# Kernel tuning notes

Measured on AMD Instinct MI355X. Metric: run time of the kernel, lower is better.

The kernel has to match this reference:

```python
import jax, jax.numpy as jnp
import numpy as np

B, T, I, H, L = 128, 2048, 4, 400, 20


def setup_inputs() -> dict:
    key = jax.random.key(0)
    ks = jax.random.split(key, 18)
    p = lambda k, shape: (jax.random.normal(k, shape, jnp.float32) * 0.05)
    return {
        "x": jax.random.normal(ks[0], (B, T, I), jnp.float32),
        "eps": jax.random.normal(ks[1], (B, L), jnp.float32),
        # encoder LSTM (input 4 -> hidden 400); torch gate order i,f,g,o; b = b_ih+b_hh
        "W_enc_ih": p(ks[2], (4 * H, I)),
        "W_enc_hh": p(ks[3], (4 * H, H)),
        "b_enc": p(ks[4], (4 * H,)),
        "W_mu": p(ks[5], (L, H)), "b_mu": p(ks[6], (L,)),
        "W_lv": p(ks[7], (L, H)), "b_lv": p(ks[8], (L,)),
        # latent -> decoder initial hidden (decoder hidden size = I = 4)
        "W_l2h": p(ks[9], (I, L)), "b_l2h": p(ks[10], (I,)),
        # input_to_hidden: 4 -> 400
        "W_i2h": p(ks[11], (H, I)), "b_i2h": p(ks[12], (H,)),
        # decoder LSTM (input 400 -> hidden 4)
        "W_dec_ih": p(ks[13], (4 * I, H)),
        "W_dec_hh": p(ks[14], (4 * I, I)),
        "b_dec": p(ks[15], (4 * I,)),
    }


def _lstm_last(xw, W_hh, h0, c0):
    # xw: [B, T, 4Hd] precomputed input-to-gate projections (+bias)
    def step(carry, xw_t):
        h, c = carry
        g = xw_t + h @ W_hh.T
        i, f, gg, o = jnp.split(g, 4, axis=-1)
        c = jax.nn.sigmoid(f) * c + jax.nn.sigmoid(i) * jnp.tanh(gg)
        h = jax.nn.sigmoid(o) * jnp.tanh(c)
        return (h, c), None
    (h, c), _ = jax.lax.scan(step, (h0, c0), jnp.swapaxes(xw, 0, 1))
    return h


def reference(x, eps, W_enc_ih, W_enc_hh, b_enc, W_mu, b_mu, W_lv, b_lv,
              W_l2h, b_l2h, W_i2h, b_i2h, W_dec_ih, W_dec_hh, b_dec):
    b = x.shape[0]
    # ---- encode ----
    xw = jnp.einsum('bti,gi->btg', x, W_enc_ih) + b_enc  # [B,T,4H]
    h0 = jnp.zeros((b, H), x.dtype)
    last = _lstm_last(xw, W_enc_hh, h0, h0)              # [B,H] == lstm_out[:, -1]
    mu = last @ W_mu.T + b_mu                            # [B,L]
    logvar = last @ W_lv.T + b_lv                        # [B,L]
    # ---- reparameterize ----
    z = mu + eps * jnp.exp(0.5 * logvar)                 # [B,L]
    # ---- decode (teacher-forced per-step loop -> fused scan) ----
    u = jax.nn.relu(jnp.einsum('bti,hi->bth', x, W_i2h) + b_i2h)  # [B,T,H]
    uw = jnp.einsum('bth,gh->btg', u, W_dec_ih) + b_dec            # [B,T,4I]
    hd0 = z @ W_l2h.T + b_l2h                                      # [B,I]
    cd0 = jnp.zeros((b, I), x.dtype)
    sample = _lstm_last(uw, W_dec_hh, hd0, cd0)                    # [B,I] last-step output
    return sample, mu, logvar
```

## Files before the change

kernel.cpp:

```cpp
#include <hip/hip_runtime.h>
#include <cstdint>

#define T_STEPS 2048
#define BPG 16
#define HROW 416
#define KCH 13
#define NPOS (128 * 2048)
#define POLL_CAP 16384

typedef float f32x4 __attribute__((ext_vector_type(4)));
typedef short s16x8 __attribute__((ext_vector_type(8)));
typedef unsigned int u32x4 __attribute__((ext_vector_type(4)));

__device__ __forceinline__ unsigned int f2bf(float f) {
  unsigned int u = __float_as_uint(f);
  return (u + 0x7FFFu + ((u >> 16) & 1u)) >> 16;
}
__device__ __forceinline__ float sigm(float x) { return 1.0f / (1.0f + __expf(-x)); }
__device__ __forceinline__ float tanh_f(float x) { return 1.0f - 2.0f / (__expf(2.0f * x) + 1.0f); }

#define DPPF(x, ctrl) __int_as_float(__builtin_amdgcn_update_dpp(0, __float_as_int(x), (ctrl), 0xf, 0xf, true))

__device__ __forceinline__ float gate_update(const f32x4 m, const int q, float& c_st) {
  const bool q0 = (q & 1), q1b = (q & 2);
  float sA = DPPF(q0 ? m[0] : m[1], 0xB1);
  float sB = DPPF(q0 ? m[2] : m[3], 0xB1);
  float n0 = q0 ? sA : m[0];
  float n1 = q0 ? m[1] : sA;
  float n2 = q0 ? sB : m[2];
  float n3 = q0 ? m[3] : sB;
  float tA = DPPF(q1b ? n0 : n2, 0x4E);
  float tB = DPPF(q1b ? n1 : n3, 0x4E);
  float g0 = q1b ? tA : n0;
  float g1 = q1b ? tB : n1;
  float g2 = q1b ? n2 : tA;
  float g3 = q1b ? n3 : tB;
  float cn = sigm(g1) * c_st + sigm(g0) * tanh_f(g2);
  c_st = cn;
  return sigm(g3) * tanh_f(cn);
}

__device__ __forceinline__ void st_sys_b128(void* p, u32x4 v) {
  asm volatile("global_store_dwordx4 %0, %1, off sc0 sc1" :: "v"(p), "v"(v) : "memory");
}

__global__ __launch_bounds__(320, 2) void enc_uw_kernel(
    const float* __restrict__ x, const float* __restrict__ W_hh,
    const float* __restrict__ W_ih, const float* __restrict__ b_enc,
    unsigned short* __restrict__ hbuf, float* __restrict__ last_h,
    int* __restrict__ ctrl,
    const float* __restrict__ W_i2h, const float* __restrict__ b_i2h,
    const float* __restrict__ W_dec, const float* __restrict__ b_dec,
    float* __restrict__ uw)
{
  __shared__ char smem[33664];
  const int tid = threadIdx.x;
  const int bid = blockIdx.x;

  if (bid >= 80) {
    float4* Wi = (float4*)smem;
    float4 (*WdT)[4] = (float4(*)[4])(smem + 6400);
    float* bi = (float*)(smem + 32000);
    float* bd = (float*)(smem + 33600);
    for (int i = tid; i < 400; i += 320) {
      Wi[i] = *(const float4*)(W_i2h + (size_t)i * 4);
      bi[i] = b_i2h[i];
    }
    for (int i = tid; i < 6400; i += 320) {
      int gq = i & 15, hh = i >> 4;
      ((float*)&WdT[hh][0])[gq] = W_dec[(size_t)gq * 400 + hh];
    }
    if (tid < 16) bd[tid] = b_dec[tid];
    __syncthreads();
#pragma unroll
    for (int rep = 0; rep < 2; ++rep) {
      const int pos = (bid - 80) * 640 + rep * 320 + tid;
      if (pos < NPOS) {
        float4 xv = *(const float4*)(x + (size_t)pos * 4);
        float a[16];
#pragma unroll
        for (int qq = 0; qq < 16; ++qq) a[qq] = bd[qq];
        for (int hh = 0; hh < 400; ++hh) {
          float4 wv = Wi[hh];
          float u = fmaxf(wv.x * xv.x + wv.y * xv.y + wv.z * xv.z + wv.w * xv.w + bi[hh], 0.f);
#pragma unroll
          for (int q4 = 0; q4 < 4; ++q4) {
            float4 d = WdT[hh][q4];
            a[q4 * 4 + 0] = fmaf(d.x, u, a[q4 * 4 + 0]);
            a[q4 * 4 + 1] = fmaf(d.y, u, a[q4 * 4 + 1]);
            a[q4 * 4 + 2] = fmaf(d.z, u, a[q4 * 4 + 2]);
            a[q4 * 4 + 3] = fmaf(d.w, u, a[q4 * 4 + 3]);
          }
        }
        float4* o = (float4*)(uw + (size_t)pos * 16);
#pragma unroll
        for (int q4 = 0; q4 < 4; ++q4)
          o[q4] = make_float4(a[q4 * 4], a[q4 * 4 + 1], a[q4 * 4 + 2], a[q4 * 4 + 3]);
      }
    }
    return;
  }

  const int g = bid & 7, s = bid >> 3;
  const int wave = tid >> 6, lane = tid & 63;
  const int bbase = g * BPG;
  const int o = s * 5 + wave;
  const int cw = lane & 15, kgrp = lane >> 4;
  const int q = lane & 3, a = (lane >> 2) & 3;
  const int gate = cw & 3, uloc = cw >> 2;
  const int ubase = 8 * o;
  const int batch = 4 * kgrp + q;
  int* tagsG = ctrl + g * 64;

  const int perm[8] = {0, 4, 1, 5, 2, 6, 3, 7};
  s16x8 bv0[KCH], bv1[KCH];
#pragma unroll
  for (int tt = 0; tt < 2; ++tt) {
    const int row = gate * 400 + ubase + tt * 4 + uloc;
    const float* wr = W_hh + (size_t)row * 400;
#pragma unroll
    for (int kc = 0; kc < KCH; ++kc) {
      s16x8 bb;
#pragma unroll
      for (int i = 0; i < 8; ++i) {
        const int gk = kc * 32 + kgrp * 8 + i;
        float w;
        if (gk < 400)      w = wr[(size_t)(kc * 4 + kgrp) * 8 + perm[i]];
        else if (gk < 404) w = W_ih[(size_t)row * 4 + (gk - 400)];
        else               w = 0.f;
        bb[i] = (short)f2bf(w);
      }
      if (tt == 0) bv0[kc] = bb; else bv1[kc] = bb;
    }
  }
  const float bias0 = b_enc[gate * 400 + ubase + uloc];
  const float bias1 = b_enc[gate * 400 + ubase + 4 + uloc];

  if (s == 0 && wave == 0 && a == 0) {
    float4 xv = *(const float4*)(x + (size_t)(bbase + batch) * T_STEPS * 4);
    u32x4 xp = {f2bf(xv.x) | (f2bf(xv.y) << 16), f2bf(xv.z) | (f2bf(xv.w) << 16), 0u, 0u};
    st_sys_b128((char*)(hbuf + (size_t)(bbase + batch) * HROW) + 800, xp);
  }
  asm volatile("s_waitcnt vmcnt(0)" ::: "memory");
  __syncthreads();
  if (wave == 0 && lane == 0)
    __hip_atomic_store(&tagsG[s], 1, __ATOMIC_RELAXED, __HIP_MEMORY_SCOPE_AGENT);

  float c0 = 0.f, c1 = 0.f;

  for (int t = 0; t < T_STEPS; ++t) {
    const int p = t & 1;
    float4 xn;
    const bool do_x = (s == 0) && (wave == 0) && (a == 0) && (t + 1 < T_STEPS);
    if (do_x) xn = *(const float4*)(x + ((size_t)(bbase + batch) * T_STEPS + (t + 1)) * 4);

    {
      const int tgt = t + 1;
      const unsigned long long* tp = (const unsigned long long*)tagsG;
      int iter = 0;
      bool ok;
      do {
        unsigned long long v = ~0ull;
        if (lane < 5)
          v = __hip_atomic_load(&tp[lane], __ATOMIC_RELAXED, __HIP_MEMORY_SCOPE_AGENT);
        ok = (lane >= 5) || (((int)(unsigned int)v >= tgt) && ((int)(v >> 32) >= tgt));
        if (++iter > POLL_CAP) break;
      } while (!__all(ok));
    }

    {
      char* dst = smem + p * 13312;
      const char* src = (const char*)(hbuf + ((size_t)p * 128 + bbase) * HROW);
      const int i0 = tid, i1 = tid + 320, i2 = tid + 640;
      const int r0 = i0 / 52, col0 = i0 % 52;
      const int r1 = i1 / 52, col1 = i1 % 52;
      const int r2 = i2 / 52, col2 = i2 % 52;
      const bool h2 = i2 < 832;
      u32x4 v0, v1, v2;
      asm volatile("global_load_dwordx4 %0, %1, off sc0 sc1"
                   : "=v"(v0) : "v"(src + r0 * 832 + col0 * 16) : "memory");
      asm volatile("global_load_dwordx4 %0, %1, off sc0 sc1"
                   : "=v"(v1) : "v"(src + r1 * 832 + col1 * 16) : "memory");
      if (h2)
        asm volatile("global_load_dwordx4 %0, %1, off sc0 sc1"
                     : "=v"(v2) : "v"(src + r2 * 832 + col2 * 16) : "memory");
      asm volatile("s_waitcnt vmcnt(0)" ::: "memory");
      *(u32x4*)(dst + r0 * 832 + col0 * 16) = v0;
      *(u32x4*)(dst + r1 * 832 + col1 * 16) = v1;
      if (h2) *(u32x4*)(dst + r2 * 832 + col2 * 16) = v2;
    }
    __syncthreads();

    const char* At = smem + p * 13312 + cw * 832 + kgrp * 16;
    s16x8 av[KCH];
#pragma unroll
    for (int kc = 0; kc < KCH; ++kc) av[kc] = *(const s16x8*)(At + kc * 64);

    f32x4 acc00 = {bias0, bias0, bias0, bias0};
    f32x4 acc01 = {0.f, 0.f, 0.f, 0.f};
    f32x4 acc10 = {bias1, bias1, bias1, bias1};
    f32x4 acc11 = {0.f, 0.f, 0.f, 0.f};
#define MM(i)                                                                    \
    if ((i) & 1) {                                                               \
      acc01 = __builtin_amdgcn_mfma_f32_16x16x32_bf16(av[i], bv0[i], acc01, 0, 0, 0); \
      acc11 = __builtin_amdgcn_mfma_f32_16x16x32_bf16(av[i], bv1[i], acc11, 0, 0, 0); \
    } else {                                                                     \
      acc00 = __builtin_amdgcn_mfma_f32_16x16x32_bf16(av[i], bv0[i], acc00, 0, 0, 0); \
      acc10 = __builtin_amdgcn_mfma_f32_16x16x32_bf16(av[i], bv1[i], acc10, 0, 0, 0); \
    }
    MM(0) MM(1) MM(2) MM(3) MM(4) MM(5) MM(6) MM(7) MM(8) MM(9) MM(10) MM(11) MM(12)
#undef MM
    f32x4 m0 = acc00 + acc01;
    f32x4 m1 = acc10 + acc11;

    float hn0 = gate_update(m0, q, c0);
    float hn1 = gate_update(m1, q, c1);

    unsigned int v32 = f2bf(hn0) | (f2bf(hn1) << 16);
    const int srcb = lane & 51;
    unsigned int w0 = (unsigned int)__shfl((int)v32, srcb);
    unsigned int w1 = (unsigned int)__shfl((int)v32, srcb + 4);
    unsigned int w2 = (unsigned int)__shfl((int)v32, srcb + 8);
    unsigned int w3 = (unsigned int)__shfl((int)v32, srcb + 12);
    if (a == 0) {
      char* rp = (char*)(hbuf + ((size_t)(p ^ 1) * 128 + bbase + batch) * HROW) + o * 16;
      u32x4 val = {w0, w1, w2, w3};
      st_sys_b128(rp, val);
      if (do_x) {
        u32x4 xp = {f2bf(xn.x) | (f2bf(xn.y) << 16), f2bf(xn.z) | (f2bf(xn.w) << 16), 0u, 0u};
        st_sys_b128(rp - o * 16 + 800, xp);
      }
    }
    if (t == T_STEPS - 1) {
      float* lp = last_h + (size_t)(bbase + batch) * 400 + ubase;
      lp[a] = hn0;
      lp[4 + a] = hn1;
    }
    asm volatile("s_waitcnt vmcnt(0)" ::: "memory");
    __syncthreads();
    if (wave == 0 && lane == 0)
      __hip_atomic_store(&tagsG[s], t + 2, __ATOMIC_RELAXED, __HIP_MEMORY_SCOPE_AGENT);
  }
}

__global__ __launch_bounds__(64) void head_dec_kernel(
    const float* __restrict__ last_h, const float* __restrict__ eps,
    const float* __restrict__ W_mu, const float* __restrict__ b_mu,
    const float* __restrict__ W_lv, const float* __restrict__ b_lv,
    const float* __restrict__ W_l2h, const float* __restrict__ b_l2h,
    const float* __restrict__ Whh, const float* __restrict__ uw,
    float* __restrict__ out)
{
  const int b = blockIdx.x, tid = threadIdx.x;
  __shared__ float smu[20], slv[20], sz[20], hd4[4];
  const float4* h4 = (const float4*)(last_h + (size_t)b * 400);
  if (tid < 40) {
    const int o = tid % 20;
    const float4* w4 = (const float4*)((tid < 20 ? W_mu : W_lv) + (size_t)o * 400);
    float s = 0.f;
#pragma unroll 4
    for (int k = 0; k < 100; ++k) {
      float4 a = h4[k], w = w4[k];
      s += a.x * w.x + a.y * w.y + a.z * w.z + a.w * w.w;
    }
    if (tid < 20) { s += b_mu[o]; smu[o] = s; out[512 + b * 20 + o] = s; }
    else          { s += b_lv[o]; slv[o] = s; out[512 + 2560 + b * 20 + o] = s; }
  }
  __syncthreads();
  if (tid < 20) sz[tid] = smu[tid] + eps[b * 20 + tid] * __expf(0.5f * slv[tid]);
  __syncthreads();
  if (tid < 4) {
    float s = b_l2h[tid];
    for (int l = 0; l < 20; ++l) s += W_l2h[tid * 20 + l] * sz[l];
    hd4[tid] = s;
  }
  __syncthreads();
  if (tid < 4) {
    const int j = tid;
    float w[4][4];
#pragma unroll
    for (int gq = 0; gq < 4; ++gq)
#pragma unroll
      for (int k = 0; k < 4; ++k)
        w[gq][k] = Whh[(gq * 4 + j) * 4 + k];
    float h = hd4[j], c = 0.f;
    const float* up = uw + (size_t)b * T_STEPS * 16 + j;
    float pn[4][4];
#pragma unroll
    for (int ss = 0; ss < 4; ++ss) {
      const float* u2 = up + (size_t)ss * 16;
      pn[ss][0] = u2[0]; pn[ss][1] = u2[4]; pn[ss][2] = u2[8]; pn[ss][3] = u2[12];
    }
    for (int tb = 0; tb < T_STEPS; tb += 4) {
#pragma unroll
      for (int ss = 0; ss < 4; ++ss) {
        float c0g = pn[ss][0], c1g = pn[ss][1], c2g = pn[ss][2], c3g = pn[ss][3];
        const int tn = tb + ss + 4;
        if (tn < T_STEPS) {
          const float* u2 = up + (size_t)tn * 16;
          pn[ss][0] = u2[0]; pn[ss][1] = u2[4]; pn[ss][2] = u2[8]; pn[ss][3] = u2[12];
        }
        float h0 = DPPF(h, 0x00), h1 = DPPF(h, 0x55), h2 = DPPF(h, 0xAA), h3 = DPPF(h, 0xFF);
        c0g += w[0][0] * h0 + w[0][1] * h1 + w[0][2] * h2 + w[0][3] * h3;
        c1g += w[1][0] * h0 + w[1][1] * h1 + w[1][2] * h2 + w[1][3] * h3;
        c2g += w[2][0] * h0 + w[2][1] * h1 + w[2][2] * h2 + w[2][3] * h3;
        c3g += w[3][0] * h0 + w[3][1] * h1 + w[3][2] * h2 + w[3][3] * h3;
        c = sigm(c1g) * c + sigm(c0g) * tanh_f(c2g);
        h = sigm(c3g) * tanh_f(c);
      }
    }
    out[b * 4 + j] = h;
  }
}

extern "C" void kernel_launch(void* const* d_in, const int* in_sizes, int n_in,
                              void* d_out, int out_size, void* d_ws, size_t ws_size,
                              hipStream_t stream)
{
  (void)in_sizes; (void)n_in; (void)out_size; (void)ws_size;
  const float* x        = (const float*)d_in[0];
  const float* eps      = (const float*)d_in[1];
  const float* W_enc_ih = (const float*)d_in[2];
  const float* W_enc_hh = (const float*)d_in[3];
  const float* b_enc    = (const float*)d_in[4];
  const float* W_mu     = (const float*)d_in[5];
  const float* b_mu     = (const float*)d_in[6];
  const float* W_lv     = (const float*)d_in[7];
  const float* b_lv     = (const float*)d_in[8];
  const float* W_l2h    = (const float*)d_in[9];
  const float* b_l2h    = (const float*)d_in[10];
  const float* W_i2h    = (const float*)d_in[11];
  const float* b_i2h    = (const float*)d_in[12];
  const float* W_dec_ih = (const float*)d_in[13];
  const float* W_dec_hh = (const float*)d_in[14];
  const float* b_dec    = (const float*)d_in[15];
  float* out = (float*)d_out;
  char* ws = (char*)d_ws;
  int* ctrl = (int*)ws;
  unsigned short* hbuf = (unsigned short*)(ws + 16384);
  float* last_h = (float*)(ws + 229376);
  float* uw = (float*)(ws + 524288);

  hipMemsetAsync(ws, 0, 229376, stream);
  enc_uw_kernel<<<490, 320, 0, stream>>>(
      x, W_enc_hh, W_enc_ih, b_enc, hbuf, last_h, ctrl,
      W_i2h, b_i2h, W_dec_ih, b_dec, uw);
  head_dec_kernel<<<128, 64, 0, stream>>>(
      last_h, eps, W_mu, b_mu, W_lv, b_lv, W_l2h, b_l2h, W_dec_hh, uw, out);
}
```

Measured before the change: 6.121 ms.

## Replace per-block tag flags with step-stamped hidden-state chunks

```diff
diff --git a/kernel.cpp b/kernel.cpp
--- a/kernel.cpp
+++ b/kernel.cpp
@@ -3,10 +3,11 @@
 
 #define T_STEPS 2048
 #define BPG 16
-#define HROW 416
+#define GROW 1216
+#define LROW 1304
 #define KCH 13
-#define NPOS (128 * 2048)
-#define POLL_CAP 16384
+#define NCHUNK (16*152)
+#define NPOS (128*2048)
 
 typedef float f32x4 __attribute__((ext_vector_type(4)));
 typedef short s16x8 __attribute__((ext_vector_type(8)));
@@ -40,20 +41,22 @@
   return sigm(g3) * tanh_f(cn);
 }
 
-__device__ __forceinline__ void st_sys_b128(void* p, u32x4 v) {
-  asm volatile("global_store_dwordx4 %0, %1, off sc0 sc1" :: "v"(p), "v"(v) : "memory");
-}
-
-__global__ __launch_bounds__(320, 2) void enc_uw_kernel(
+__device__ __forceinline__ void st_sys_b64(void* p, unsigned long long v) {
+  asm volatile("global_store_dwordx2 %0, %1, off sc0 sc1" :: "v"(p), "v"(v) : "memory");
+}
+__device__ __forceinline__ unsigned long long mk2(unsigned int w0, unsigned int w1) {
+  return (unsigned long long)w0 | ((unsigned long long)w1 << 32);
+}
+
+__global__ __launch_bounds__(320, 1) void enc_uw_kernel(
     const float* __restrict__ x, const float* __restrict__ W_hh,
     const float* __restrict__ W_ih, const float* __restrict__ b_enc,
-    unsigned short* __restrict__ hbuf, float* __restrict__ last_h,
-    int* __restrict__ ctrl,
+    char* __restrict__ hb, float* __restrict__ last_h,
     const float* __restrict__ W_i2h, const float* __restrict__ b_i2h,
     const float* __restrict__ W_dec, const float* __restrict__ b_dec,
     float* __restrict__ uw)
 {
-  __shared__ char smem[33664];
+  __shared__ char smem[41792];
   const int tid = threadIdx.x;
   const int bid = blockIdx.x;
 
@@ -110,9 +113,7 @@
   const int gate = cw & 3, uloc = cw >> 2;
   const int ubase = 8 * o;
   const int batch = 4 * kgrp + q;
-  int* tagsG = ctrl + g * 64;
-
-  const int perm[8] = {0, 4, 1, 5, 2, 6, 3, 7};
+
   s16x8 bv0[KCH], bv1[KCH];
 #pragma unroll
   for (int tt = 0; tt < 2; ++tt) {
@@ -125,7 +126,7 @@
       for (int i = 0; i < 8; ++i) {
         const int gk = kc * 32 + kgrp * 8 + i;
         float w;
-        if (gk < 400)      w = wr[(size_t)(kc * 4 + kgrp) * 8 + perm[i]];
+        if (gk < 400)      w = wr[gk];
         else if (gk < 404) w = W_ih[(size_t)row * 4 + (gk - 400)];
         else               w = 0.f;
         bb[i] = (short)f2bf(w);
@@ -136,110 +137,150 @@
   const float bias0 = b_enc[gate * 400 + ubase + uloc];
   const float bias1 = b_enc[gate * 400 + ubase + 4 + uloc];
 
-  if (s == 0 && wave == 0 && a == 0) {
-    float4 xv = *(const float4*)(x + (size_t)(bbase + batch) * T_STEPS * 4);
-    u32x4 xp = {f2bf(xv.x) | (f2bf(xv.y) << 16), f2bf(xv.z) | (f2bf(xv.w) << 16), 0u, 0u};
-    st_sys_b128((char*)(hbuf + (size_t)(bbase + batch) * HROW) + 800, xp);
-  }
-  asm volatile("s_waitcnt vmcnt(0)" ::: "memory");
-  __syncthreads();
-  if (wave == 0 && lane == 0)
-    __hip_atomic_store(&tagsG[s], 1, __ATOMIC_RELAXED, __HIP_MEMORY_SCOPE_AGENT);
-
-  float c0 = 0.f, c1 = 0.f;
+  {
+    if (a < 3) {
+      unsigned int w1 = (a == 2) ? 1u : (1u << 16);
+      st_sys_b64(hb + (size_t)(bbase + batch) * GROW + (3 * o + a) * 8, mk2(0u, w1));
+    }
+    if (s == 0 && wave == 0 && a == 0) {
+      float4 xv = *(const float4*)(x + (size_t)(bbase + batch) * T_STEPS * 4);
+      char* rb = hb + (size_t)(bbase + batch) * GROW;
+      st_sys_b64(rb + 150 * 8, mk2(f2bf(xv.x) | (f2bf(xv.y) << 16), f2bf(xv.z) | (1u << 16)));
+      st_sys_b64(rb + 151 * 8, mk2(f2bf(xv.w), 1u << 16));
+    }
+    asm volatile("s_waitcnt expcnt(0)" ::: "memory");
+  }
+
+  int goffs[8], loffs[8];
+  bool valid[8], typ2[8];
+#pragma unroll
+  for (int k = 0; k < 8; ++k) {
+    int ci = tid + 320 * k;
+    valid[k] = (ci < NCHUNK);
+    int cc = valid[k] ? ci : 0;
+    int r = cc / 152, c = cc - r * 152;
+    goffs[k] = r * GROW + c * 8;
+    loffs[k] = r * LROW + c * 8;
+    typ2[k] = ((c % 3) == 2);
+  }
+
+  int* flags = (int*)(smem + 41728);
+  float cs0 = 0.f, cs1 = 0.f;
+  int budget = 150000;
 
   for (int t = 0; t < T_STEPS; ++t) {
     const int p = t & 1;
+    const char* gb = hb + (size_t)(p * 128 + bbase) * GROW;
+    char* lb = smem + p * 20864;
+
     float4 xn;
     const bool do_x = (s == 0) && (wave == 0) && (a == 0) && (t + 1 < T_STEPS);
     if (do_x) xn = *(const float4*)(x + ((size_t)(bbase + batch) * T_STEPS + (t + 1)) * 4);
 
-    {
-      const int tgt = t + 1;
-      const unsigned long long* tp = (const unsigned long long*)tagsG;
-      int iter = 0;
-      bool ok;
-      do {
-        unsigned long long v = ~0ull;
-        if (lane < 5)
-          v = __hip_atomic_load(&tp[lane], __ATOMIC_RELAXED, __HIP_MEMORY_SCOPE_AGENT);
-        ok = (lane >= 5) || (((int)(unsigned int)v >= tgt) && ((int)(v >> 32) >= tgt));
-        if (++iter > POLL_CAP) break;
-      } while (!__all(ok));
-    }
-
-    {
-      char* dst = smem + p * 13312;
-      const char* src = (const char*)(hbuf + ((size_t)p * 128 + bbase) * HROW);
-      const int i0 = tid, i1 = tid + 320, i2 = tid + 640;
-      const int r0 = i0 / 52, col0 = i0 % 52;
-      const int r1 = i1 / 52, col1 = i1 % 52;
-      const int r2 = i2 / 52, col2 = i2 % 52;
-      const bool h2 = i2 < 832;
-      u32x4 v0, v1, v2;
-      asm volatile("global_load_dwordx4 %0, %1, off sc0 sc1"
-                   : "=v"(v0) : "v"(src + r0 * 832 + col0 * 16) : "memory");
-      asm volatile("global_load_dwordx4 %0, %1, off sc0 sc1"
-                   : "=v"(v1) : "v"(src + r1 * 832 + col1 * 16) : "memory");
-      if (h2)
-        asm volatile("global_load_dwordx4 %0, %1, off sc0 sc1"
-                     : "=v"(v2) : "v"(src + r2 * 832 + col2 * 16) : "memory");
+    const unsigned int st = (unsigned int)(t + 1) & 0xffffu;
+
+    for (;;) {
+      unsigned long long v0, v1, v2, v3, v4, v5, v6, v7;
+#define LDC(i)                                                                  \
+      asm volatile("global_load_dwordx2 %0, %1, off sc0 sc1"                    \
+                   : "=v"(v##i) : "v"(gb + goffs[i]) : "memory");
+      LDC(0) LDC(1) LDC(2) LDC(3) LDC(4) LDC(5) LDC(6)
+      if (valid[7]) LDC(7)
+#undef LDC
       asm volatile("s_waitcnt vmcnt(0)" ::: "memory");
-      *(u32x4*)(dst + r0 * 832 + col0 * 16) = v0;
-      *(u32x4*)(dst + r1 * 832 + col1 * 16) = v1;
-      if (h2) *(u32x4*)(dst + r2 * 832 + col2 * 16) = v2;
-    }
-    __syncthreads();
-
-    const char* At = smem + p * 13312 + cw * 832 + kgrp * 16;
-    s16x8 av[KCH];
-#pragma unroll
-    for (int kc = 0; kc < KCH; ++kc) av[kc] = *(const s16x8*)(At + kc * 64);
-
+      bool ok = true;
+#define CHK(i)                                                                  \
+      {                                                                          \
+        unsigned int w1 = (unsigned int)(v##i >> 32);                            \
+        unsigned int sp = typ2[i] ? (w1 & 0xffffu) : (w1 >> 16);                 \
+        ok &= (sp == st);                                                        \
+        *(unsigned long long*)(lb + loffs[i]) = v##i;                            \
+      }
+      CHK(0) CHK(1) CHK(2) CHK(3) CHK(4) CHK(5) CHK(6)
+      if (valid[7]) CHK(7)
+#undef CHK
+      const bool okw = __all(ok);
+      if (lane == 0) flags[wave] = okw ? (t + 1) : -1;
+      __syncthreads();
+      const int tv = t + 1;
+      bool all5 = (flags[0] == tv) & (flags[1] == tv) & (flags[2] == tv) &
+                  (flags[3] == tv) & (flags[4] == tv);
+      if (all5) break;
+      if (--budget < 0) break;
+      __syncthreads();
+    }
+
+    if (do_x) {
+      const unsigned int st2 = (unsigned int)(t + 2) & 0xffffu;
+      char* rb = hb + (size_t)((p ^ 1) * 128 + bbase + batch) * GROW;
+      st_sys_b64(rb + 150 * 8, mk2(f2bf(xn.x) | (f2bf(xn.y) << 16), f2bf(xn.z) | (st2 << 16)));
+      st_sys_b64(rb + 151 * 8, mk2(f2bf(xn.w), st2 << 16));
+    }
+
+    const char* lbr = lb + cw * LROW;
     f32x4 acc00 = {bias0, bias0, bias0, bias0};
     f32x4 acc01 = {0.f, 0.f, 0.f, 0.f};
     f32x4 acc10 = {bias1, bias1, bias1, bias1};
     f32x4 acc11 = {0.f, 0.f, 0.f, 0.f};
-#define MM(i)                                                                    \
-    if ((i) & 1) {                                                               \
-      acc01 = __builtin_amdgcn_mfma_f32_16x16x32_bf16(av[i], bv0[i], acc01, 0, 0, 0); \
-      acc11 = __builtin_amdgcn_mfma_f32_16x16x32_bf16(av[i], bv1[i], acc11, 0, 0, 0); \
-    } else {                                                                     \
-      acc00 = __builtin_amdgcn_mfma_f32_16x16x32_bf16(av[i], bv0[i], acc00, 0, 0, 0); \
-      acc10 = __builtin_amdgcn_mfma_f32_16x16x32_bf16(av[i], bv1[i], acc10, 0, 0, 0); \
-    }
-    MM(0) MM(1) MM(2) MM(3) MM(4) MM(5) MM(6) MM(7) MM(8) MM(9) MM(10) MM(11) MM(12)
-#undef MM
+#pragma unroll
+    for (int kc = 0; kc < KCH; ++kc) {
+      const char* cp = lbr + (4 * kc + kgrp) * 24;
+      unsigned long long d01 = *(const unsigned long long*)cp;
+      unsigned long long d23 = *(const unsigned long long*)(cp + 8);
+      unsigned long long d45 = *(const unsigned long long*)(cp + 16);
+      unsigned int w0 = (unsigned int)d01, w1 = (unsigned int)(d01 >> 32);
+      unsigned int w2 = (unsigned int)d23, w3 = (unsigned int)(d23 >> 32);
+      unsigned int w4 = (unsigned int)d45;
+      unsigned int a01 = w0;
+      unsigned int a23 = (w1 & 0xffffu) | (w2 << 16);
+      unsigned int a45 = (w2 >> 16) | (w3 << 16);
+      unsigned int a67 = w4;
+      if (kc == KCH - 1 && kgrp >= 2) {
+        a45 = 0u; a67 = 0u;
+        if (kgrp == 3) { a01 = 0u; a23 = 0u; }
+      }
+      union { u32x4 u; s16x8 s; } cvt;
+      cvt.u = (u32x4){a01, a23, a45, a67};
+      const s16x8 av = cvt.s;
+      if (kc & 1) {
+        acc01 = __builtin_amdgcn_mfma_f32_16x16x32_bf16(av, bv0[kc], acc01, 0, 0, 0);
+        acc11 = __builtin_amdgcn_mfma_f32_16x16x32_bf16(av, bv1[kc], acc11, 0, 0, 0);
+      } else {
+        acc00 = __builtin_amdgcn_mfma_f32_16x16x32_bf16(av, bv0[kc], acc00, 0, 0, 0);
+        acc10 = __builtin_amdgcn_mfma_f32_16x16x32_bf16(av, bv1[kc], acc10, 0, 0, 0);
+      }
+    }
     f32x4 m0 = acc00 + acc01;
     f32x4 m1 = acc10 + acc11;
 
-    float hn0 = gate_update(m0, q, c0);
-    float hn1 = gate_update(m1, q, c1);
-
-    unsigned int v32 = f2bf(hn0) | (f2bf(hn1) << 16);
-    const int srcb = lane & 51;
-    unsigned int w0 = (unsigned int)__shfl((int)v32, srcb);
-    unsigned int w1 = (unsigned int)__shfl((int)v32, srcb + 4);
-    unsigned int w2 = (unsigned int)__shfl((int)v32, srcb + 8);
-    unsigned int w3 = (unsigned int)__shfl((int)v32, srcb + 12);
-    if (a == 0) {
-      char* rp = (char*)(hbuf + ((size_t)(p ^ 1) * 128 + bbase + batch) * HROW) + o * 16;
-      u32x4 val = {w0, w1, w2, w3};
-      st_sys_b128(rp, val);
-      if (do_x) {
-        u32x4 xp = {f2bf(xn.x) | (f2bf(xn.y) << 16), f2bf(xn.z) | (f2bf(xn.w) << 16), 0u, 0u};
-        st_sys_b128(rp - o * 16 + 800, xp);
-      }
+    float hn0 = gate_update(m0, q, cs0);
+    float hn1 = gate_update(m1, q, cs1);
+
+    const int hb0 = (int)f2bf(hn0), hb1 = (int)f2bf(hn1);
+    const int base = lane & 51;
+    unsigned int g0 = (unsigned int)__shfl(hb0, base);
+    unsigned int g1 = (unsigned int)__shfl(hb0, base + 4);
+    unsigned int g2 = (unsigned int)__shfl(hb0, base + 8);
+    unsigned int g3 = (unsigned int)__shfl(hb0, base + 12);
+    unsigned int h0 = (unsigned int)__shfl(hb1, base);
+    unsigned int h1 = (unsigned int)__shfl(hb1, base + 4);
+    unsigned int h2 = (unsigned int)__shfl(hb1, base + 8);
+    unsigned int h3 = (unsigned int)__shfl(hb1, base + 12);
+    if (a < 3) {
+      const unsigned int st2 = (unsigned int)(t + 2) & 0xffffu;
+      unsigned int w0, w1;
+      if (a == 0)      { w0 = g0 | (g1 << 16); w1 = g2 | (st2 << 16); }
+      else if (a == 1) { w0 = g3 | (h0 << 16); w1 = h1 | (st2 << 16); }
+      else             { w0 = h2 | (h3 << 16); w1 = st2; }
+      st_sys_b64(hb + (size_t)((p ^ 1) * 128 + bbase + batch) * GROW + (3 * o + a) * 8,
+                 mk2(w0, w1));
     }
     if (t == T_STEPS - 1) {
       float* lp = last_h + (size_t)(bbase + batch) * 400 + ubase;
       lp[a] = hn0;
       lp[4 + a] = hn1;
     }
-    asm volatile("s_waitcnt vmcnt(0)" ::: "memory");
-    __syncthreads();
-    if (wave == 0 && lane == 0)
-      __hip_atomic_store(&tagsG[s], t + 2, __ATOMIC_RELAXED, __HIP_MEMORY_SCOPE_AGENT);
+    asm volatile("s_waitcnt expcnt(0)" ::: "memory");
   }
 }
 
@@ -336,14 +377,13 @@
   const float* b_dec    = (const float*)d_in[15];
   float* out = (float*)d_out;
   char* ws = (char*)d_ws;
-  int* ctrl = (int*)ws;
-  unsigned short* hbuf = (unsigned short*)(ws + 16384);
-  float* last_h = (float*)(ws + 229376);
+  char* hb = ws;
+  float* last_h = (float*)(ws + 311296);
   float* uw = (float*)(ws + 524288);
 
-  hipMemsetAsync(ws, 0, 229376, stream);
+  hipMemsetAsync(ws, 0, 311296, stream);
   enc_uw_kernel<<<490, 320, 0, stream>>>(
-      x, W_enc_hh, W_enc_ih, b_enc, hbuf, last_h, ctrl,
+      x, W_enc_hh, W_enc_ih, b_enc, hb, last_h,
       W_i2h, b_i2h, W_dec_ih, b_dec, uw);
   head_dec_kernel<<<128, 64, 0, stream>>>(
       last_h, eps, W_mu, b_mu, W_lv, b_lv, W_l2h, b_l2h, W_dec_hh, uw, out);
```

New measurement: 11.34 ms. 85.3% more time.

## Use per-wave step flags and direct global A-loads instead of block barriers

Applied to the files above, without the earlier changes.

```diff
diff --git a/kernel.cpp b/kernel.cpp
--- a/kernel.cpp
+++ b/kernel.cpp
@@ -3,10 +3,9 @@
 
 #define T_STEPS 2048
 #define BPG 16
-#define HROW 416
+#define GROWB 832
 #define KCH 13
-#define NPOS (128 * 2048)
-#define POLL_CAP 16384
+#define NPOS (128*2048)
 
 typedef float f32x4 __attribute__((ext_vector_type(4)));
 typedef short s16x8 __attribute__((ext_vector_type(8)));
@@ -44,10 +43,10 @@
   asm volatile("global_store_dwordx4 %0, %1, off sc0 sc1" :: "v"(p), "v"(v) : "memory");
 }
 
-__global__ __launch_bounds__(320, 2) void enc_uw_kernel(
+__global__ __launch_bounds__(320, 1) void enc_uw_kernel(
     const float* __restrict__ x, const float* __restrict__ W_hh,
     const float* __restrict__ W_ih, const float* __restrict__ b_enc,
-    unsigned short* __restrict__ hbuf, float* __restrict__ last_h,
+    char* __restrict__ hb, float* __restrict__ last_h,
     int* __restrict__ ctrl,
     const float* __restrict__ W_i2h, const float* __restrict__ b_i2h,
     const float* __restrict__ W_dec, const float* __restrict__ b_dec,
@@ -110,7 +109,7 @@
   const int gate = cw & 3, uloc = cw >> 2;
   const int ubase = 8 * o;
   const int batch = 4 * kgrp + q;
-  int* tagsG = ctrl + g * 64;
+  int* tagsG = ctrl + g * 256;
 
   const int perm[8] = {0, 4, 1, 5, 2, 6, 3, 7};
   s16x8 bv0[KCH], bv1[KCH];
@@ -139,17 +138,19 @@
   if (s == 0 && wave == 0 && a == 0) {
     float4 xv = *(const float4*)(x + (size_t)(bbase + batch) * T_STEPS * 4);
     u32x4 xp = {f2bf(xv.x) | (f2bf(xv.y) << 16), f2bf(xv.z) | (f2bf(xv.w) << 16), 0u, 0u};
-    st_sys_b128((char*)(hbuf + (size_t)(bbase + batch) * HROW) + 800, xp);
+    st_sys_b128(hb + (size_t)(bbase + batch) * GROWB + 800, xp);
   }
   asm volatile("s_waitcnt vmcnt(0)" ::: "memory");
-  __syncthreads();
-  if (wave == 0 && lane == 0)
-    __hip_atomic_store(&tagsG[s], 1, __ATOMIC_RELAXED, __HIP_MEMORY_SCOPE_AGENT);
-
-  float c0 = 0.f, c1 = 0.f;
+  if (lane == 0)
+    __hip_atomic_store(&tagsG[o], 1, __ATOMIC_RELAXED, __HIP_MEMORY_SCOPE_AGENT);
+
+  float cs0 = 0.f, cs1 = 0.f;
+  int budget = 4000000;
 
   for (int t = 0; t < T_STEPS; ++t) {
     const int p = t & 1;
+    const char* gb = hb + (size_t)(p * 128 + bbase) * GROWB;
+
     float4 xn;
     const bool do_x = (s == 0) && (wave == 0) && (a == 0) && (t + 1 < T_STEPS);
     if (do_x) xn = *(const float4*)(x + ((size_t)(bbase + batch) * T_STEPS + (t + 1)) * 4);
@@ -157,73 +158,73 @@
     {
       const int tgt = t + 1;
       const unsigned long long* tp = (const unsigned long long*)tagsG;
-      int iter = 0;
       bool ok;
       do {
         unsigned long long v = ~0ull;
-        if (lane < 5)
+        if (lane < 25)
           v = __hip_atomic_load(&tp[lane], __ATOMIC_RELAXED, __HIP_MEMORY_SCOPE_AGENT);
-        ok = (lane >= 5) || (((int)(unsigned int)v >= tgt) && ((int)(v >> 32) >= tgt));
-        if (++iter > POLL_CAP) break;
+        ok = (lane >= 25) || (((int)(unsigned int)v >= tgt) && ((int)(v >> 32) >= tgt));
+        if (--budget < 0) break;
       } while (!__all(ok));
     }
 
-    {
-      char* dst = smem + p * 13312;
-      const char* src = (const char*)(hbuf + ((size_t)p * 128 + bbase) * HROW);
-      const int i0 = tid, i1 = tid + 320, i2 = tid + 640;
-      const int r0 = i0 / 52, col0 = i0 % 52;
-      const int r1 = i1 / 52, col1 = i1 % 52;
-      const int r2 = i2 / 52, col2 = i2 % 52;
-      const bool h2 = i2 < 832;
-      u32x4 v0, v1, v2;
-      asm volatile("global_load_dwordx4 %0, %1, off sc0 sc1"
-                   : "=v"(v0) : "v"(src + r0 * 832 + col0 * 16) : "memory");
-      asm volatile("global_load_dwordx4 %0, %1, off sc0 sc1"
-                   : "=v"(v1) : "v"(src + r1 * 832 + col1 * 16) : "memory");
-      if (h2)
-        asm volatile("global_load_dwordx4 %0, %1, off sc0 sc1"
-                     : "=v"(v2) : "v"(src + r2 * 832 + col2 * 16) : "memory");
-      asm volatile("s_waitcnt vmcnt(0)" ::: "memory");
-      *(u32x4*)(dst + r0 * 832 + col0 * 16) = v0;
-      *(u32x4*)(dst + r1 * 832 + col1 * 16) = v1;
-      if (h2) *(u32x4*)(dst + r2 * 832 + col2 * 16) = v2;
-    }
-    __syncthreads();
-
-    const char* At = smem + p * 13312 + cw * 832 + kgrp * 16;
-    s16x8 av[KCH];
-#pragma unroll
-    for (int kc = 0; kc < KCH; ++kc) av[kc] = *(const s16x8*)(At + kc * 64);
+    const char* Ab = gb + cw * GROWB + kgrp * 16;
+    s16x8 av0, av1, av2, av3, av4, av5, av6, av7, av8, av9, av10, av11, av12;
+    asm volatile(
+        "global_load_dwordx4 %0, %13, off sc0 sc1\n\t"
+        "global_load_dwordx4 %1, %13, off offset:64 sc0 sc1\n\t"
+        "global_load_dwordx4 %2, %13, off offset:128 sc0 sc1\n\t"
+        "global_load_dwordx4 %3, %13, off offset:192 sc0 sc1\n\t"
+        "global_load_dwordx4 %4, %13, off offset:256 sc0 sc1\n\t"
+        "global_load_dwordx4 %5, %13, off offset:320 sc0 sc1\n\t"
+        "global_load_dwordx4 %6, %13, off offset:384 sc0 sc1\n\t"
+        "global_load_dwordx4 %7, %13, off offset:448 sc0 sc1\n\t"
+        "global_load_dwordx4 %8, %13, off offset:512 sc0 sc1\n\t"
+        "global_load_dwordx4 %9, %13, off offset:576 sc0 sc1\n\t"
+        "global_load_dwordx4 %10, %13, off offset:640 sc0 sc1\n\t"
+        "global_load_dwordx4 %11, %13, off offset:704 sc0 sc1\n\t"
+        "global_load_dwordx4 %12, %13, off offset:768 sc0 sc1\n\t"
+        "s_waitcnt vmcnt(0)"
+        : "=&v"(av0), "=&v"(av1), "=&v"(av2), "=&v"(av3), "=&v"(av4),
+          "=&v"(av5), "=&v"(av6), "=&v"(av7), "=&v"(av8), "=&v"(av9),
+          "=&v"(av10), "=&v"(av11), "=&v"(av12)
+        : "v"(Ab)
+        : "memory");
+    __builtin_amdgcn_sched_barrier(0);
 
     f32x4 acc00 = {bias0, bias0, bias0, bias0};
     f32x4 acc01 = {0.f, 0.f, 0.f, 0.f};
     f32x4 acc10 = {bias1, bias1, bias1, bias1};
     f32x4 acc11 = {0.f, 0.f, 0.f, 0.f};
-#define MM(i)                                                                    \
+#define MM(av, i)                                                                \
     if ((i) & 1) {                                                               \
-      acc01 = __builtin_amdgcn_mfma_f32_16x16x32_bf16(av[i], bv0[i], acc01, 0, 0, 0); \
-      acc11 = __builtin_amdgcn_mfma_f32_16x16x32_bf16(av[i], bv1[i], acc11, 0, 0, 0); \
+      acc01 = __builtin_amdgcn_mfma_f32_16x16x32_bf16(av, bv0[i], acc01, 0, 0, 0); \
+      acc11 = __builtin_amdgcn_mfma_f32_16x16x32_bf16(av, bv1[i], acc11, 0, 0, 0); \
     } else {                                                                     \
-      acc00 = __builtin_amdgcn_mfma_f32_16x16x32_bf16(av[i], bv0[i], acc00, 0, 0, 0); \
-      acc10 = __builtin_amdgcn_mfma_f32_16x16x32_bf16(av[i], bv1[i], acc10, 0, 0, 0); \
-    }
-    MM(0) MM(1) MM(2) MM(3) MM(4) MM(5) MM(6) MM(7) MM(8) MM(9) MM(10) MM(11) MM(12)
+      acc00 = __builtin_amdgcn_mfma_f32_16x16x32_bf16(av, bv0[i], acc00, 0, 0, 0); \
+      acc10 = __builtin_amdgcn_mfma_f32_16x16x32_bf16(av, bv1[i], acc10, 0, 0, 0); \
+    }
+    MM(av0, 0) MM(av1, 1) MM(av2, 2) MM(av3, 3) MM(av4, 4) MM(av5, 5) MM(av6, 6)
+    MM(av7, 7) MM(av8, 8) MM(av9, 9) MM(av10, 10) MM(av11, 11) MM(av12, 12)
 #undef MM
     f32x4 m0 = acc00 + acc01;
     f32x4 m1 = acc10 + acc11;
 
-    float hn0 = gate_update(m0, q, c0);
-    float hn1 = gate_update(m1, q, c1);
-
-    unsigned int v32 = f2bf(hn0) | (f2bf(hn1) << 16);
-    const int srcb = lane & 51;
-    unsigned int w0 = (unsigned int)__shfl((int)v32, srcb);
-    unsigned int w1 = (unsigned int)__shfl((int)v32, srcb + 4);
-    unsigned int w2 = (unsigned int)__shfl((int)v32, srcb + 8);
-    unsigned int w3 = (unsigned int)__shfl((int)v32, srcb + 12);
+    float hn0 = gate_update(m0, q, cs0);
+    float hn1 = gate_update(m1, q, cs1);
+
+    const int hb0 = (int)f2bf(hn0), hb1 = (int)f2bf(hn1);
+    const int base = lane & 51;
+    unsigned int w0 = (unsigned int)__shfl(hb0, base) |
+                      ((unsigned int)__shfl(hb1, base) << 16);
+    unsigned int w1 = (unsigned int)__shfl(hb0, base + 4) |
+                      ((unsigned int)__shfl(hb1, base + 4) << 16);
+    unsigned int w2 = (unsigned int)__shfl(hb0, base + 8) |
+                      ((unsigned int)__shfl(hb1, base + 8) << 16);
+    unsigned int w3 = (unsigned int)__shfl(hb0, base + 12) |
+                      ((unsigned int)__shfl(hb1, base + 12) << 16);
     if (a == 0) {
-      char* rp = (char*)(hbuf + ((size_t)(p ^ 1) * 128 + bbase + batch) * HROW) + o * 16;
+      char* rp = hb + (size_t)((p ^ 1) * 128 + bbase + batch) * GROWB + o * 16;
       u32x4 val = {w0, w1, w2, w3};
       st_sys_b128(rp, val);
       if (do_x) {
@@ -237,9 +238,8 @@
       lp[4 + a] = hn1;
     }
     asm volatile("s_waitcnt vmcnt(0)" ::: "memory");
-    __syncthreads();
-    if (wave == 0 && lane == 0)
-      __hip_atomic_store(&tagsG[s], t + 2, __ATOMIC_RELAXED, __HIP_MEMORY_SCOPE_AGENT);
+    if (lane == 0)
+      __hip_atomic_store(&tagsG[o], t + 2, __ATOMIC_RELAXED, __HIP_MEMORY_SCOPE_AGENT);
   }
 }
 
@@ -337,13 +337,13 @@
   float* out = (float*)d_out;
   char* ws = (char*)d_ws;
   int* ctrl = (int*)ws;
-  unsigned short* hbuf = (unsigned short*)(ws + 16384);
+  char* hb = ws + 16384;
   float* last_h = (float*)(ws + 229376);
   float* uw = (float*)(ws + 524288);
 
   hipMemsetAsync(ws, 0, 229376, stream);
   enc_uw_kernel<<<490, 320, 0, stream>>>(
-      x, W_enc_hh, W_enc_ih, b_enc, hbuf, last_h, ctrl,
+      x, W_enc_hh, W_enc_ih, b_enc, hb, last_h, ctrl,
       W_i2h, b_i2h, W_dec_ih, b_dec, uw);
   head_dec_kernel<<<128, 64, 0, stream>>>(
       last_h, eps, W_mu, b_mu, W_lv, b_lv, W_l2h, b_l2h, W_dec_hh, uw, out);
```

New measurement: 11.19 ms. 82.8% more time.
